# Kernel tuning notes

Measured on AMD Instinct MI355X. Metric: run time of the kernel, lower is better.

The kernel has to match this reference:

```python
import jax, jax.numpy as jnp
import numpy as np

ALPHA = 0.25
GAMMA = 2.0
FG_W = 13.0
BG_W = 1.0
DS = 8  # downsample_factor: boxes are in original image coords, masks at feature res


def setup_inputs() -> dict:
    key = jax.random.key(0)
    k1, k2, k3, k4 = jax.random.split(key, 4)
    B, N, C, H, W, M = 2, 6, 81, 112, 200, 20
    depth_logits = jax.random.normal(k1, (B, N, C, H, W), dtype=jnp.float32)
    depth_target = jax.random.randint(k2, (B, N, H, W), 0, C, dtype=jnp.int32)
    # (x, y, w, h) boxes in original image coords (~1600x900)
    xy = jax.random.uniform(k3, (B, N, M, 2)) * jnp.array([1400.0, 700.0], jnp.float32)
    wh = 20.0 + jax.random.uniform(k4, (B, N, M, 2)) * 180.0
    gt_bboxes_2d = jnp.concatenate([xy, wh], axis=-1).astype(jnp.float32)
    return {"depth_logits": depth_logits, "depth_target": depth_target,
            "gt_bboxes_2d": gt_bboxes_2d}


def _focal_loss(logits, target):
    # logits [BN, C, H, W], target [BN, H, W] -> per-pixel focal loss [BN, H, W]
    log_p = jax.nn.log_softmax(logits, axis=1)
    log_pt = jnp.take_along_axis(log_p, target[:, None].astype(jnp.int32), axis=1)[:, 0]
    pt = jnp.exp(log_pt)
    return -ALPHA * (1.0 - pt) ** GAMMA * log_pt


def _fg_mask(boxes, H, W):
    # boxes [BN, M, 4] = (x, y, w, h); rectangle fill at feature resolution
    x, y, w, h = boxes[..., 0], boxes[..., 1], boxes[..., 2], boxes[..., 3]
    u1 = jnp.floor(x / DS)
    v1 = jnp.floor(y / DS)
    u2 = jnp.ceil((x + w) / DS)
    v2 = jnp.ceil((y + h) / DS)
    xs = jnp.arange(W, dtype=jnp.float32)
    ys = jnp.arange(H, dtype=jnp.float32)
    in_x = (xs[None, None, :] >= u1[..., None]) & (xs[None, None, :] < u2[..., None])  # [BN,M,W]
    in_y = (ys[None, None, :] >= v1[..., None]) & (ys[None, None, :] < v2[..., None])  # [BN,M,H]
    return jnp.any(in_y[:, :, :, None] & in_x[:, :, None, :], axis=1)  # [BN,H,W]


def reference(depth_logits, depth_target, gt_bboxes_2d):
    B, N, C, H, W = depth_logits.shape
    logits = depth_logits.reshape(B * N, C, H, W)
    target = depth_target.reshape(B * N, H, W)
    loss = _focal_loss(logits, target)  # [BN, H, W]

    fg = _fg_mask(gt_bboxes_2d.reshape(B * N, -1, 4), H, W)
    bg = ~fg
    weights = jnp.where(fg, FG_W, BG_W).astype(loss.dtype)
    num_pixels = jnp.asarray(fg.size, loss.dtype)  # fg.sum() + bg.sum() == total pixels

    wloss = loss * weights
    fg_loss = jnp.where(fg, wloss, 0.0).sum() / num_pixels
    bg_loss = jnp.where(bg, wloss, 0.0).sum() / num_pixels
    return fg_loss + bg_loss
```

## Files before the change

kernel.cpp:

```cpp
#include <hip/hip_runtime.h>
#include <math.h>

namespace {
constexpr int Cc = 81, Hc = 112, Wc = 200, Mc = 20;
constexpr int BN   = 12;
constexpr int HW   = Hc * Wc;
constexpr int NPIX = BN * HW;
constexpr int PPB  = 128;
constexpr int TPB  = 256;
constexpr int NBLK = NPIX / PPB;
constexpr float kAlpha = 0.25f;
constexpr float kFgW   = 13.0f;
constexpr float kBgW   = 1.0f;
constexpr float kInvDS = 0.125f;
}

__global__ __launch_bounds__(TPB) void ddn_pass1(
    const float* __restrict__ logits,
    const int*   __restrict__ target,
    const float* __restrict__ boxes,
    float*       __restrict__ partial)
{
    __shared__ float sh[PPB];
    __shared__ float wsum[4];

    const int t    = threadIdx.x;
    const int pl   = t & (PPB - 1);
    const int half = t >> 7;
    const int pixb = blockIdx.x * PPB;
    const int bn   = pixb / HW;
    const int hw   = pixb - bn * HW + pl;
    const int pix  = pixb + pl;

    const float* basebn = logits + (size_t)bn * Cc * HW + hw;
    const float* base   = basebn + (size_t)(half * 40) * HW;

    float acc = 0.f;
    float v[16];
    #pragma unroll
    for (int b = 0; b < 2; ++b) {
        #pragma unroll
        for (int j = 0; j < 16; ++j)
            v[j] = base[(size_t)(b * 16 + j) * HW];
        #pragma unroll
        for (int j = 0; j < 16; ++j)
            acc += __expf(v[j]);
    }
    #pragma unroll
    for (int j = 0; j < 8; ++j)
        v[j] = base[(size_t)(32 + j) * HW];
    #pragma unroll
    for (int j = 0; j < 8; ++j)
        acc += __expf(v[j]);

    float xt = 0.f;
    if (half == 0) {
        const int tgt = target[pix];
        xt   = basebn[(size_t)tgt * HW];
        acc += __expf(basebn[(size_t)80 * HW]);
    } else {
        sh[pl] = acc;
    }
    __syncthreads();

    float local = 0.f;
    if (half == 0) {
        const float s    = acc + sh[pl];
        const float lpt  = xt - __logf(s);
        const float om   = 1.f - __expf(lpt);
        const float loss = -kAlpha * om * om * lpt;

        const int h = hw / Wc;
        const int w = hw - h * Wc;
        const float hf = (float)h, wf = (float)w;
        const float* bx = boxes + (size_t)bn * Mc * 4;
        bool fg = false;
        #pragma unroll
        for (int m = 0; m < Mc; ++m) {
            const float bxx = bx[m * 4 + 0];
            const float bxy = bx[m * 4 + 1];
            const float u1 = floorf(bxx * kInvDS);
            const float v1 = floorf(bxy * kInvDS);
            const float u2 = ceilf((bxx + bx[m * 4 + 2]) * kInvDS);
            const float v2 = ceilf((bxy + bx[m * 4 + 3]) * kInvDS);
            fg |= (hf >= v1) & (hf < v2) & (wf >= u1) & (wf < u2);
        }
        local = loss * (fg ? kFgW : kBgW);
    }

    #pragma unroll
    for (int off = 32; off > 0; off >>= 1)
        local += __shfl_down(local, off, 64);
    if ((t & 63) == 0) wsum[t >> 6] = local;
    __syncthreads();
    if (t == 0)
        partial[blockIdx.x] = wsum[0] + wsum[1] + wsum[2] + wsum[3];
}

__global__ __launch_bounds__(1024) void ddn_pass2(
    const float* __restrict__ partial, float* __restrict__ out)
{
    const int t = threadIdx.x;
    float s = 0.f;
    for (int i = t; i < NBLK; i += 1024)
        s += partial[i];
    #pragma unroll
    for (int off = 32; off > 0; off >>= 1)
        s += __shfl_down(s, off, 64);
    __shared__ float smem[16];
    if ((t & 63) == 0) smem[t >> 6] = s;
    __syncthreads();
    if (t < 64) {
        float z = (t < 16) ? smem[t] : 0.f;
        #pragma unroll
        for (int off = 8; off > 0; off >>= 1)
            z += __shfl_down(z, off, 64);
        if (t == 0) out[0] = z * (1.0f / (float)NPIX);
    }
}

extern "C" void kernel_launch(void* const* d_in, const int* in_sizes, int n_in,
                              void* d_out, int out_size, void* d_ws, size_t ws_size,
                              hipStream_t stream) {
    const float* logits = (const float*)d_in[0];
    const int*   target = (const int*)d_in[1];
    const float* boxes  = (const float*)d_in[2];
    float* out     = (float*)d_out;
    float* partial = (float*)d_ws;

    ddn_pass1<<<NBLK, TPB, 0, stream>>>(logits, target, boxes, partial);
    ddn_pass2<<<1, 1024, 0, stream>>>(partial, out);
}
```

Before: 23.95 us.

## Use float4 loads with a four-way channel split over 256 pixels per block

Each block now covers 256 pixels, and each of its four waves sums exp over a 20-channel slice (wave 3 also takes the last channel) using float4 loads of 4 adjacent pixels. The per-wave partial sums go through shared memory, after which each thread finishes one pixel's loss and foreground test. This replaces scalar loads and two-way splitting with wider, more coalesced memory transactions and spreads the epilogue across all threads. The trade-offs are half as many blocks, more shared memory, and a float4 load path that depends on HW being a multiple of 4 so rows stay aligned.

```diff
diff --git a/kernel.cpp b/kernel.cpp
--- a/kernel.cpp
+++ b/kernel.cpp
@@ -6,7 +6,7 @@
 constexpr int BN   = 12;
 constexpr int HW   = Hc * Wc;
 constexpr int NPIX = BN * HW;
-constexpr int PPB  = 128;
+constexpr int PPB  = 256;
 constexpr int TPB  = 256;
 constexpr int NBLK = NPIX / PPB;
 constexpr float kAlpha = 0.25f;
@@ -21,72 +21,71 @@
     const float* __restrict__ boxes,
     float*       __restrict__ partial)
 {
-    __shared__ float sh[PPB];
+    __shared__ float sh[4][PPB];
     __shared__ float wsum[4];
 
     const int t    = threadIdx.x;
-    const int pl   = t & (PPB - 1);
-    const int half = t >> 7;
+    const int lane = t & 63;
+    const int wv   = t >> 6;
     const int pixb = blockIdx.x * PPB;
-    const int bn   = pixb / HW;
-    const int hw   = pixb - bn * HW + pl;
-    const int pix  = pixb + pl;
 
-    const float* basebn = logits + (size_t)bn * Cc * HW + hw;
-    const float* base   = basebn + (size_t)(half * 40) * HW;
+    const int  epix = pixb + t;
+    const int  ebn  = epix / HW;
+    const int  ehw  = epix - ebn * HW;
+    const int  etgt = target[epix];
+    const float xt  = logits[(size_t)ebn * Cc * HW + (size_t)etgt * HW + ehw];
 
-    float acc = 0.f;
-    float v[16];
+    const int qpix = pixb + lane * 4;
+    const int qbn  = qpix / HW;
+    const int qhw  = qpix - qbn * HW;
+    const float4* lp4 = reinterpret_cast<const float4*>(
+        logits + (size_t)qbn * Cc * HW + qhw);
+    const int c0 = wv * 20;
+
+    float a0 = 0.f, a1 = 0.f, a2 = 0.f, a3 = 0.f;
+    float4 v[10];
     #pragma unroll
     for (int b = 0; b < 2; ++b) {
         #pragma unroll
-        for (int j = 0; j < 16; ++j)
-            v[j] = base[(size_t)(b * 16 + j) * HW];
+        for (int j = 0; j < 10; ++j)
+            v[j] = lp4[(size_t)(c0 + b * 10 + j) * (HW / 4)];
         #pragma unroll
-        for (int j = 0; j < 16; ++j)
-            acc += __expf(v[j]);
+        for (int j = 0; j < 10; ++j) {
+            a0 += __expf(v[j].x);
+            a1 += __expf(v[j].y);
+            a2 += __expf(v[j].z);
+            a3 += __expf(v[j].w);
+        }
     }
-    #pragma unroll
-    for (int j = 0; j < 8; ++j)
-        v[j] = base[(size_t)(32 + j) * HW];
-    #pragma unroll
-    for (int j = 0; j < 8; ++j)
-        acc += __expf(v[j]);
-
-    float xt = 0.f;
-    if (half == 0) {
-        const int tgt = target[pix];
-        xt   = basebn[(size_t)tgt * HW];
-        acc += __expf(basebn[(size_t)80 * HW]);
-    } else {
-        sh[pl] = acc;
+    if (wv == 3) {
+        const float4 u = lp4[(size_t)80 * (HW / 4)];
+        a0 += __expf(u.x); a1 += __expf(u.y);
+        a2 += __expf(u.z); a3 += __expf(u.w);
     }
+    reinterpret_cast<float4*>(sh[wv])[lane] = make_float4(a0, a1, a2, a3);
     __syncthreads();
 
-    float local = 0.f;
-    if (half == 0) {
-        const float s    = acc + sh[pl];
-        const float lpt  = xt - __logf(s);
-        const float om   = 1.f - __expf(lpt);
-        const float loss = -kAlpha * om * om * lpt;
+    const float s    = sh[0][t] + sh[1][t] + sh[2][t] + sh[3][t];
+    const float lpt  = xt - __logf(s);
+    const float om   = 1.f - __expf(lpt);
+    const float loss = -kAlpha * om * om * lpt;
 
-        const int h = hw / Wc;
-        const int w = hw - h * Wc;
-        const float hf = (float)h, wf = (float)w;
-        const float* bx = boxes + (size_t)bn * Mc * 4;
-        bool fg = false;
-        #pragma unroll
-        for (int m = 0; m < Mc; ++m) {
-            const float bxx = bx[m * 4 + 0];
-            const float bxy = bx[m * 4 + 1];
-            const float u1 = floorf(bxx * kInvDS);
-            const float v1 = floorf(bxy * kInvDS);
-            const float u2 = ceilf((bxx + bx[m * 4 + 2]) * kInvDS);
-            const float v2 = ceilf((bxy + bx[m * 4 + 3]) * kInvDS);
-            fg |= (hf >= v1) & (hf < v2) & (wf >= u1) & (wf < u2);
-        }
-        local = loss * (fg ? kFgW : kBgW);
+    const int h = ehw / Wc;
+    const int w = ehw - h * Wc;
+    const float hf = (float)h, wf = (float)w;
+    const float* bx = boxes + (size_t)ebn * Mc * 4;
+    bool fg = false;
+    #pragma unroll
+    for (int m = 0; m < Mc; ++m) {
+        const float bxx = bx[m * 4 + 0];
+        const float bxy = bx[m * 4 + 1];
+        const float u1 = floorf(bxx * kInvDS);
+        const float v1 = floorf(bxy * kInvDS);
+        const float u2 = ceilf((bxx + bx[m * 4 + 2]) * kInvDS);
+        const float v2 = ceilf((bxy + bx[m * 4 + 3]) * kInvDS);
+        fg |= (hf >= v1) & (hf < v2) & (wf >= u1) & (wf < u2);
     }
+    float local = loss * (fg ? kFgW : kBgW);
 
     #pragma unroll
     for (int off = 32; off > 0; off >>= 1)
```

After: 23.47 us. 2.0% less time.
